# Kernel tuning notes

Hardware: AMD Instinct MI355X
Metric: run time of the kernel (lower is better)

Reference implementation:

```python
import jax, jax.numpy as jnp
import numpy as np

BATCH, NUM_MASKS, IN_DIM, OUT_DIM = 512, 16, 1024, 1024


def setup_inputs() -> dict:
    key = jax.random.key(0)
    k1, k2, k3 = jax.random.split(key, 3)
    x = jax.random.normal(k1, (BATCH, NUM_MASKS, IN_DIM), dtype=jnp.float32)
    kernel = jax.random.normal(k2, (IN_DIM, OUT_DIM), dtype=jnp.float32) * (1.0 / np.sqrt(IN_DIM))
    masks = jax.random.uniform(k3, (NUM_MASKS, IN_DIM, OUT_DIM), dtype=jnp.float32)
    return {"x": x, "kernel": kernel, "masks": masks}


def reference(x, kernel, masks):
    # masked_kernel[m, i, o] = kernel[i, o] * masks[m, i, o]
    masked_kernel = kernel[None, :, :] * masks  # (M, I, O)
    # Original tf.scan serializes batch; equivalent math is one batched einsum:
    # out[b, m, o] = sum_i x[b, m, i] * masked_kernel[m, i, o]
    # NOTE: the executed tf.scan path applies NO activation, so neither do we.
    out = jnp.einsum('bmi,mio->bmo', x, masked_kernel)  # (B, M, O)
    return out
```

## Files before the change

kernel.cpp:

```cpp
#include <hip/hip_runtime.h>
#include <hip/hip_bf16.h>


#define BATCH 512
#define NMASK 16
#define IN_D  1024
#define OUT_D 1024

#define BM 128
#define BN 128
#define BK 32
#define NT (IN_D / BK)
#define AKP 40
#define BKP 34
#define THREADS 512

using bf16x8  = __attribute__((ext_vector_type(8))) __bf16;
using bf16x4t = __attribute__((ext_vector_type(4))) __bf16;
using f32x4   = __attribute__((ext_vector_type(4))) float;
using f32x2   = __attribute__((ext_vector_type(2))) float;
using u16x8   = __attribute__((ext_vector_type(8))) unsigned short;
using u16x4   = __attribute__((ext_vector_type(4))) unsigned short;

__device__ __forceinline__ unsigned short f2bf(float f) {
    unsigned u = __float_as_uint(f);
    u += 0x7fffu + ((u >> 16) & 1u);
    return (unsigned short)(u >> 16);
}

__global__ void __launch_bounds__(THREADS, 4)
mdl_mfma_kernel(const float* __restrict__ X,
                const float* __restrict__ Kn,
                const float* __restrict__ Mk,
                float* __restrict__ Out)
{
    __shared__ __align__(16) unsigned short As[2][BM * AKP];
    __shared__ __align__(16) unsigned short Bs[2][BN * BKP];

    const int t = threadIdx.x;
    const int l = t & 63;
    const int w = t >> 6;

    const int raw = blockIdx.x;
    const int wg  = (raw & 7) * 64 + (raw >> 3);
    const int m   = wg >> 5;
    const int ob  = (wg >> 2) & 7;
    const int bb  = wg & 3;

    const int wr = w >> 2;
    const int wc = w & 3;

    f32x4 acc[4][2];
#pragma unroll
    for (int mi = 0; mi < 4; ++mi)
#pragma unroll
        for (int ni = 0; ni < 2; ++ni)
            acc[mi][ni] = (f32x4){0.f, 0.f, 0.f, 0.f};

    const int a_row = t >> 2;
    const int a_k   = (t & 3) * 8;
    const int o_l = (t & 63) * 2;
    const int ig  = t >> 6;
    const int i_l = ig * 4;

    const float* Xa  = X + ((size_t)(bb * BM + a_row) * NMASK + m) * IN_D + a_k;
    const float* Knb = Kn + (size_t)i_l * OUT_D + ob * BN + o_l;
    const float* Mkb = Mk + ((size_t)m * IN_D + i_l) * OUT_D + ob * BN + o_l;

    f32x4 av0, av1;
    f32x2 kv[4], mv[4];

    auto LOAD = [&](int kt) {
        av0 = *(const f32x4*)(Xa + kt);
        av1 = *(const f32x4*)(Xa + kt + 4);
#pragma unroll
        for (int r = 0; r < 4; ++r) {
            kv[r] = *(const f32x2*)(Knb + (size_t)(kt + r) * OUT_D);
            mv[r] = *(const f32x2*)(Mkb + (size_t)(kt + r) * OUT_D);
        }
    };

    auto STORE = [&](int buf) {
        u16x8 va;
#pragma unroll
        for (int j = 0; j < 4; ++j) { va[j] = f2bf(av0[j]); va[4 + j] = f2bf(av1[j]); }
        *(u16x8*)(&As[buf][a_row * AKP + a_k]) = va;
#pragma unroll
        for (int c = 0; c < 2; ++c) {
            u16x4 v;
#pragma unroll
            for (int r = 0; r < 4; ++r) v[r] = f2bf(kv[r][c] * mv[r][c]);
            *(u16x4*)(&Bs[buf][(o_l + c) * BKP + ig * 4]) = v;
        }
    };

    auto MFMA_PHASE = [&](int buf) {
        const int kg = (l >> 4) * 8;
        bf16x8 af[4], bfv[2];
#pragma unroll
        for (int mi = 0; mi < 4; ++mi) {
            const int r = wr * 64 + mi * 16 + (l & 15);
            af[mi] = *(const bf16x8*)(&As[buf][r * AKP + kg]);
        }
#pragma unroll
        for (int ni = 0; ni < 2; ++ni) {
            const int n = wc * 32 + ni * 16 + (l & 15);
            bf16x4t lo = *(const bf16x4t*)(&Bs[buf][n * BKP + kg]);
            bf16x4t hi = *(const bf16x4t*)(&Bs[buf][n * BKP + kg + 4]);
            bf16x8 f;
            f[0] = lo[0]; f[1] = lo[1]; f[2] = lo[2]; f[3] = lo[3];
            f[4] = hi[0]; f[5] = hi[1]; f[6] = hi[2]; f[7] = hi[3];
            bfv[ni] = f;
        }
#pragma unroll
        for (int mi = 0; mi < 4; ++mi)
#pragma unroll
            for (int ni = 0; ni < 2; ++ni)
                acc[mi][ni] = __builtin_amdgcn_mfma_f32_16x16x32_bf16(
                    af[mi], bfv[ni], acc[mi][ni], 0, 0, 0);
    };

    LOAD(0);
    STORE(0);
    __syncthreads();
    int cur = 0;
    for (int tt = 0; tt < NT; ++tt) {
        if (tt + 1 < NT) {
            LOAD((tt + 1) * BK);
            __builtin_amdgcn_sched_barrier(0);
        }
        MFMA_PHASE(cur);
        if (tt + 1 < NT) STORE(cur ^ 1);
        __syncthreads();
        cur ^= 1;
    }

    const int r0 = bb * BM + wr * 64 + (l >> 4) * 4;
    const int c0 = ob * BN + wc * 32 + (l & 15);
#pragma unroll
    for (int mi = 0; mi < 4; ++mi) {
#pragma unroll
        for (int j = 0; j < 4; ++j) {
            const size_t row = (size_t)(r0 + mi * 16 + j);
            float* op = Out + (row * NMASK + m) * OUT_D + c0;
#pragma unroll
            for (int ni = 0; ni < 2; ++ni)
                op[ni * 16] = acc[mi][ni][j];
        }
    }
}

extern "C" void kernel_launch(void* const* d_in, const int* in_sizes, int n_in,
                              void* d_out, int out_size, void* d_ws, size_t ws_size,
                              hipStream_t stream) {
    (void)in_sizes; (void)n_in; (void)d_ws; (void)ws_size; (void)out_size;
    const float* X  = (const float*)d_in[0];
    const float* Kn = (const float*)d_in[1];
    const float* Mk = (const float*)d_in[2];
    float* Out = (float*)d_out;

    const int nblocks = (BATCH / BM) * (OUT_D / BN) * NMASK;
    mdl_mfma_kernel<<<nblocks, THREADS, 0, stream>>>(X, Kn, Mk, Out);
}
```

Baseline: 52.34 us.

## Prefetch masked-kernel tiles two stages ahead with double register sets and lighter barriers

The global loads for the kernel and mask tiles are now issued two K-tiles ahead into alternating register sets, while X is still prefetched one tile ahead. The loop is unrolled by two so the LDS buffer indices are static. The block barrier is replaced with an explicit lgkmcnt wait plus s_barrier, and the A fragments are loaded per MFMA row instead of all at once. The aim is to hide more of the mask/kernel global-memory latency, at the cost of more VGPRs under launch_bounds(512,4), which may cause spills or reduce occupancy.

```diff
diff --git a/kernel.cpp b/kernel.cpp
--- a/kernel.cpp
+++ b/kernel.cpp
@@ -27,6 +27,8 @@
     u += 0x7fffu + ((u >> 16) & 1u);
     return (unsigned short)(u >> 16);
 }
+
+struct BRegs { f32x2 kv[4]; f32x2 mv[4]; };
 
 __global__ void __launch_bounds__(THREADS, 4)
 mdl_mfma_kernel(const float* __restrict__ X,
@@ -68,40 +70,35 @@
     const float* Mkb = Mk + ((size_t)m * IN_D + i_l) * OUT_D + ob * BN + o_l;
 
     f32x4 av0, av1;
-    f32x2 kv[4], mv[4];
+    BRegs b0, b1;
 
-    auto LOAD = [&](int kt) {
+    auto LOADA = [&](int kt) {
         av0 = *(const f32x4*)(Xa + kt);
         av1 = *(const f32x4*)(Xa + kt + 4);
+    };
+    auto LOADB = [&](BRegs& bg, int kt) {
 #pragma unroll
         for (int r = 0; r < 4; ++r) {
-            kv[r] = *(const f32x2*)(Knb + (size_t)(kt + r) * OUT_D);
-            mv[r] = *(const f32x2*)(Mkb + (size_t)(kt + r) * OUT_D);
+            bg.kv[r] = *(const f32x2*)(Knb + (size_t)(kt + r) * OUT_D);
+            bg.mv[r] = *(const f32x2*)(Mkb + (size_t)(kt + r) * OUT_D);
         }
     };
-
-    auto STORE = [&](int buf) {
+    auto STORE = [&](int buf, BRegs& bg) {
+#pragma unroll
+        for (int c = 0; c < 2; ++c) {
+            u16x4 v;
+#pragma unroll
+            for (int r = 0; r < 4; ++r) v[r] = f2bf(bg.kv[r][c] * bg.mv[r][c]);
+            *(u16x4*)(&Bs[buf][(o_l + c) * BKP + ig * 4]) = v;
+        }
         u16x8 va;
 #pragma unroll
         for (int j = 0; j < 4; ++j) { va[j] = f2bf(av0[j]); va[4 + j] = f2bf(av1[j]); }
         *(u16x8*)(&As[buf][a_row * AKP + a_k]) = va;
-#pragma unroll
-        for (int c = 0; c < 2; ++c) {
-            u16x4 v;
-#pragma unroll
-            for (int r = 0; r < 4; ++r) v[r] = f2bf(kv[r][c] * mv[r][c]);
-            *(u16x4*)(&Bs[buf][(o_l + c) * BKP + ig * 4]) = v;
-        }
     };
-
     auto MFMA_PHASE = [&](int buf) {
         const int kg = (l >> 4) * 8;
-        bf16x8 af[4], bfv[2];
-#pragma unroll
-        for (int mi = 0; mi < 4; ++mi) {
-            const int r = wr * 64 + mi * 16 + (l & 15);
-            af[mi] = *(const bf16x8*)(&As[buf][r * AKP + kg]);
-        }
+        bf16x8 bfv[2];
 #pragma unroll
         for (int ni = 0; ni < 2; ++ni) {
             const int n = wc * 32 + ni * 16 + (l & 15);
@@ -113,26 +110,41 @@
             bfv[ni] = f;
         }
 #pragma unroll
-        for (int mi = 0; mi < 4; ++mi)
+        for (int mi = 0; mi < 4; ++mi) {
+            const int r = wr * 64 + mi * 16 + (l & 15);
+            bf16x8 af = *(const bf16x8*)(&As[buf][r * AKP + kg]);
 #pragma unroll
             for (int ni = 0; ni < 2; ++ni)
                 acc[mi][ni] = __builtin_amdgcn_mfma_f32_16x16x32_bf16(
-                    af[mi], bfv[ni], acc[mi][ni], 0, 0, 0);
+                    af, bfv[ni], acc[mi][ni], 0, 0, 0);
+        }
+    };
+    auto BARRIER = [&]() {
+        asm volatile("s_waitcnt lgkmcnt(0)" ::: "memory");
+        __builtin_amdgcn_sched_barrier(0);
+        __builtin_amdgcn_s_barrier();
+        __builtin_amdgcn_sched_barrier(0);
     };
 
-    LOAD(0);
-    STORE(0);
-    __syncthreads();
-    int cur = 0;
-    for (int tt = 0; tt < NT; ++tt) {
-        if (tt + 1 < NT) {
-            LOAD((tt + 1) * BK);
-            __builtin_amdgcn_sched_barrier(0);
-        }
-        MFMA_PHASE(cur);
-        if (tt + 1 < NT) STORE(cur ^ 1);
-        __syncthreads();
-        cur ^= 1;
+    LOADA(0);
+    LOADB(b0, 0);
+    STORE(0, b0);
+    LOADB(b1, BK);
+    BARRIER();
+
+    for (int tt = 0; tt < NT; tt += 2) {
+        if (tt + 1 < NT) LOADA((tt + 1) * BK);
+        if (tt + 2 < NT) LOADB(b0, (tt + 2) * BK);
+        __builtin_amdgcn_sched_barrier(0);
+        MFMA_PHASE(0);
+        if (tt + 1 < NT) STORE(1, b1);
+        BARRIER();
+        if (tt + 2 < NT) LOADA((tt + 2) * BK);
+        if (tt + 3 < NT) LOADB(b1, (tt + 3) * BK);
+        __builtin_amdgcn_sched_barrier(0);
+        MFMA_PHASE(1);
+        if (tt + 2 < NT) STORE(0, b0);
+        BARRIER();
     }
 
     const int r0 = bb * BM + wr * 64 + (l >> 4) * 4;
```

New measurement: 56.90 us. +8.7%, slower.

## Use 256x128 tiles with 32x32x16 MFMA and XOR-swizzled LDS layout

Applied to the files above, without the earlier changes.

Doubles the batch tile to 256 rows so each block reuses the masked-kernel tile (kernel*mask product and its loads) across twice as many rows, halving mask/kernel global traffic and conversion work. Switches from 16x16x32 to 32x32x16 bf16 MFMA with 64x64 per-wave tiles, and replaces the padded B layout with an XOR-swizzled layout allowing single 16-byte LDS reads. The plain syncthreads is replaced by an explicit lgkmcnt wait plus s_barrier. Costs more registers and LDS per block and halves the grid to 256 blocks, which may reduce occupancy.

```diff
diff --git a/kernel.cpp b/kernel.cpp
--- a/kernel.cpp
+++ b/kernel.cpp
@@ -7,26 +7,18 @@
 #define IN_D  1024
 #define OUT_D 1024
 
-#define BM 128
+#define BM 256
 #define BN 128
 #define BK 32
 #define NT (IN_D / BK)
 #define AKP 40
-#define BKP 34
 #define THREADS 512
 
-using bf16x8  = __attribute__((ext_vector_type(8))) __bf16;
-using bf16x4t = __attribute__((ext_vector_type(4))) __bf16;
-using f32x4   = __attribute__((ext_vector_type(4))) float;
-using f32x2   = __attribute__((ext_vector_type(2))) float;
-using u16x8   = __attribute__((ext_vector_type(8))) unsigned short;
-using u16x4   = __attribute__((ext_vector_type(4))) unsigned short;
-
-__device__ __forceinline__ unsigned short f2bf(float f) {
-    unsigned u = __float_as_uint(f);
-    u += 0x7fffu + ((u >> 16) & 1u);
-    return (unsigned short)(u >> 16);
-}
+using bf16x8 = __attribute__((ext_vector_type(8))) __bf16;
+using bf16x4 = __attribute__((ext_vector_type(4))) __bf16;
+using f32x16 = __attribute__((ext_vector_type(16))) float;
+using f32x4  = __attribute__((ext_vector_type(4))) float;
+using f32x2  = __attribute__((ext_vector_type(2))) float;
 
 __global__ void __launch_bounds__(THREADS, 4)
 mdl_mfma_kernel(const float* __restrict__ X,
@@ -35,44 +27,48 @@
                 float* __restrict__ Out)
 {
     __shared__ __align__(16) unsigned short As[2][BM * AKP];
-    __shared__ __align__(16) unsigned short Bs[2][BN * BKP];
+    __shared__ __align__(16) unsigned short Bs[2][BN * AKP];
 
     const int t = threadIdx.x;
     const int l = t & 63;
     const int w = t >> 6;
 
     const int raw = blockIdx.x;
-    const int wg  = (raw & 7) * 64 + (raw >> 3);
-    const int m   = wg >> 5;
-    const int ob  = (wg >> 2) & 7;
-    const int bb  = wg & 3;
+    const int wg  = (raw & 7) * 32 + (raw >> 3);
+    const int m   = wg >> 4;
+    const int ob  = (wg >> 1) & 7;
+    const int bb  = wg & 1;
 
-    const int wr = w >> 2;
-    const int wc = w & 3;
+    const int wrow = (w >> 1) * 64;
+    const int wcol = (w & 1) * 64;
 
-    f32x4 acc[4][2];
+    f32x16 acc[2][2];
 #pragma unroll
-    for (int mi = 0; mi < 4; ++mi)
+    for (int ti = 0; ti < 2; ++ti)
 #pragma unroll
-        for (int ni = 0; ni < 2; ++ni)
-            acc[mi][ni] = (f32x4){0.f, 0.f, 0.f, 0.f};
+        for (int tj = 0; tj < 2; ++tj)
+#pragma unroll
+            for (int e = 0; e < 16; ++e)
+                acc[ti][tj][e] = 0.f;
 
-    const int a_row = t >> 2;
-    const int a_k   = (t & 3) * 8;
-    const int o_l = (t & 63) * 2;
-    const int ig  = t >> 6;
-    const int i_l = ig * 4;
+    const int a_row = t >> 1;
+    const int a_kh  = (t & 1) * 16;
+    const int a_x   = (a_row >> 3) & 3;
+    const int a_p0  = (t & 1) * 2;
+    const int o2  = (t & 63) * 2;
+    const int kq  = w * 4;
 
-    const float* Xa  = X + ((size_t)(bb * BM + a_row) * NMASK + m) * IN_D + a_k;
-    const float* Knb = Kn + (size_t)i_l * OUT_D + ob * BN + o_l;
-    const float* Mkb = Mk + ((size_t)m * IN_D + i_l) * OUT_D + ob * BN + o_l;
+    const float* Xa  = X + ((size_t)(bb * BM + a_row) * NMASK + m) * IN_D + a_kh;
+    const float* Knb = Kn + (size_t)kq * OUT_D + ob * BN + o2;
+    const float* Mkb = Mk + ((size_t)m * IN_D + kq) * OUT_D + ob * BN + o2;
 
-    f32x4 av0, av1;
+    f32x4 av[4];
     f32x2 kv[4], mv[4];
 
     auto LOAD = [&](int kt) {
-        av0 = *(const f32x4*)(Xa + kt);
-        av1 = *(const f32x4*)(Xa + kt + 4);
+#pragma unroll
+        for (int j = 0; j < 4; ++j)
+            av[j] = *(const f32x4*)(Xa + kt + j * 4);
 #pragma unroll
         for (int r = 0; r < 4; ++r) {
             kv[r] = *(const f32x2*)(Knb + (size_t)(kt + r) * OUT_D);
@@ -81,71 +77,89 @@
     };
 
     auto STORE = [&](int buf) {
-        u16x8 va;
-#pragma unroll
-        for (int j = 0; j < 4; ++j) { va[j] = f2bf(av0[j]); va[4 + j] = f2bf(av1[j]); }
-        *(u16x8*)(&As[buf][a_row * AKP + a_k]) = va;
 #pragma unroll
         for (int c = 0; c < 2; ++c) {
-            u16x4 v;
+            const int o  = o2 + c;
+            const int xb = (o >> 3) & 3;
+            bf16x4 v;
 #pragma unroll
-            for (int r = 0; r < 4; ++r) v[r] = f2bf(kv[r][c] * mv[r][c]);
-            *(u16x4*)(&Bs[buf][(o_l + c) * BKP + ig * 4]) = v;
+            for (int r = 0; r < 4; ++r)
+                v[r] = (__bf16)(kv[r][c] * mv[r][c]);
+            *(bf16x4*)(&Bs[buf][o * AKP + (((w >> 1) ^ xb) * 8) + (w & 1) * 4]) = v;
+        }
+        bf16x8 va0, va1;
+#pragma unroll
+        for (int j = 0; j < 4; ++j) {
+            va0[j] = (__bf16)av[0][j];  va0[4 + j] = (__bf16)av[1][j];
+            va1[j] = (__bf16)av[2][j];  va1[4 + j] = (__bf16)av[3][j];
+        }
+        *(bf16x8*)(&As[buf][a_row * AKP + ((a_p0 ^ a_x) * 8)])       = va0;
+        *(bf16x8*)(&As[buf][a_row * AKP + (((a_p0 + 1) ^ a_x) * 8)]) = va1;
+    };
+
+    auto MFMA_PHASE = [&](int buf) {
+#pragma unroll
+        for (int s = 0; s < 2; ++s) {
+            const int p = s * 2 + (l >> 5);
+            bf16x8 af[2], bfv[2];
+#pragma unroll
+            for (int ti = 0; ti < 2; ++ti) {
+                const int r  = wrow + ti * 32 + (l & 31);
+                const int xa = (r >> 3) & 3;
+                af[ti] = *(const bf16x8*)(&As[buf][r * AKP + ((p ^ xa) * 8)]);
+            }
+#pragma unroll
+            for (int tj = 0; tj < 2; ++tj) {
+                const int o  = wcol + tj * 32 + (l & 31);
+                const int xb = (o >> 3) & 3;
+                bfv[tj] = *(const bf16x8*)(&Bs[buf][o * AKP + ((p ^ xb) * 8)]);
+            }
+#pragma unroll
+            for (int ti = 0; ti < 2; ++ti)
+#pragma unroll
+                for (int tj = 0; tj < 2; ++tj)
+                    acc[ti][tj] = __builtin_amdgcn_mfma_f32_32x32x16_bf16(
+                        af[ti], bfv[tj], acc[ti][tj], 0, 0, 0);
         }
     };
 
-    auto MFMA_PHASE = [&](int buf) {
-        const int kg = (l >> 4) * 8;
-        bf16x8 af[4], bfv[2];
-#pragma unroll
-        for (int mi = 0; mi < 4; ++mi) {
-            const int r = wr * 64 + mi * 16 + (l & 15);
-            af[mi] = *(const bf16x8*)(&As[buf][r * AKP + kg]);
-        }
-#pragma unroll
-        for (int ni = 0; ni < 2; ++ni) {
-            const int n = wc * 32 + ni * 16 + (l & 15);
-            bf16x4t lo = *(const bf16x4t*)(&Bs[buf][n * BKP + kg]);
-            bf16x4t hi = *(const bf16x4t*)(&Bs[buf][n * BKP + kg + 4]);
-            bf16x8 f;
-            f[0] = lo[0]; f[1] = lo[1]; f[2] = lo[2]; f[3] = lo[3];
-            f[4] = hi[0]; f[5] = hi[1]; f[6] = hi[2]; f[7] = hi[3];
-            bfv[ni] = f;
-        }
-#pragma unroll
-        for (int mi = 0; mi < 4; ++mi)
-#pragma unroll
-            for (int ni = 0; ni < 2; ++ni)
-                acc[mi][ni] = __builtin_amdgcn_mfma_f32_16x16x32_bf16(
-                    af[mi], bfv[ni], acc[mi][ni], 0, 0, 0);
+    auto BARRIER = [&]() {
+        asm volatile("s_waitcnt lgkmcnt(0)" ::: "memory");
+        __builtin_amdgcn_sched_barrier(0);
+        __builtin_amdgcn_s_barrier();
+        __builtin_amdgcn_sched_barrier(0);
     };
 
     LOAD(0);
     STORE(0);
-    __syncthreads();
-    int cur = 0;
+    BARRIER();
+
     for (int tt = 0; tt < NT; ++tt) {
+        const int cur = tt & 1;
         if (tt + 1 < NT) {
             LOAD((tt + 1) * BK);
             __builtin_amdgcn_sched_barrier(0);
         }
         MFMA_PHASE(cur);
         if (tt + 1 < NT) STORE(cur ^ 1);
-        __syncthreads();
-        cur ^= 1;
+        BARRIER();
     }
 
-    const int r0 = bb * BM + wr * 64 + (l >> 4) * 4;
-    const int c0 = ob * BN + wc * 32 + (l & 15);
+    const int r0 = bb * BM + wrow + 4 * (l >> 5);
+    const int c0 = ob * BN + wcol + (l & 31);
 #pragma unroll
-    for (int mi = 0; mi < 4; ++mi) {
+    for (int ti = 0; ti < 2; ++ti) {
 #pragma unroll
-        for (int j = 0; j < 4; ++j) {
-            const size_t row = (size_t)(r0 + mi * 16 + j);
-            float* op = Out + (row * NMASK + m) * OUT_D + c0;
+        for (int tj = 0; tj < 2; ++tj) {
 #pragma unroll
-            for (int ni = 0; ni < 2; ++ni)
-                op[ni * 16] = acc[mi][ni][j];
+            for (int g = 0; g < 4; ++g) {
+#pragma unroll
+                for (int q = 0; q < 4; ++q) {
+                    const int row = r0 + ti * 32 + g * 8 + q;
+                    const int col = c0 + tj * 32;
+                    Out[((size_t)row * NMASK + m) * OUT_D + col] = acc[ti][tj][g * 4 + q];
+                }
+            }
         }
     }
 }
```

Measured after the change: 56.68 us. +8.3%, slower.

## Stream mask tiles via global_load_lds DMA and restructure pipeline

Applied to the files above, without the earlier changes.

Mask tiles are now copied straight from global memory into an fp32 shared-memory staging buffer with global_load_lds, double-buffered one tile ahead. X and kernel loads are issued at the start of each iteration and converted in the same iteration, so they are no longer prefetched. The masked product and bf16 conversion now read masks from LDS, and a second barrier per iteration is added. The aim is to cut vector-register pressure and issue cost for the large mask stream, at the price of 32KB of extra LDS (which may lower occupancy) and X/kernel load latency exposed inside the loop.

```diff
diff --git a/kernel.cpp b/kernel.cpp
--- a/kernel.cpp
+++ b/kernel.cpp
@@ -15,17 +15,17 @@
 #define BKP 34
 #define THREADS 512
 
-using bf16x8  = __attribute__((ext_vector_type(8))) __bf16;
-using bf16x4t = __attribute__((ext_vector_type(4))) __bf16;
-using f32x4   = __attribute__((ext_vector_type(4))) float;
-using f32x2   = __attribute__((ext_vector_type(2))) float;
-using u16x8   = __attribute__((ext_vector_type(8))) unsigned short;
-using u16x4   = __attribute__((ext_vector_type(4))) unsigned short;
+using bf16x8 = __attribute__((ext_vector_type(8))) __bf16;
+using bf16x4 = __attribute__((ext_vector_type(4))) __bf16;
+using f32x4  = __attribute__((ext_vector_type(4))) float;
+using f32x2  = __attribute__((ext_vector_type(2))) float;
 
-__device__ __forceinline__ unsigned short f2bf(float f) {
-    unsigned u = __float_as_uint(f);
-    u += 0x7fffu + ((u >> 16) & 1u);
-    return (unsigned short)(u >> 16);
+typedef const __attribute__((address_space(1))) void gvoid_t;
+typedef __attribute__((address_space(3))) void lvoid_t;
+
+__device__ __forceinline__ void dma16(const void* g, const void* l) {
+    __builtin_amdgcn_global_load_lds((gvoid_t*)(uintptr_t)g,
+                                     (lvoid_t*)(uintptr_t)l, 16, 0, 0);
 }
 
 __global__ void __launch_bounds__(THREADS, 4)
@@ -34,6 +34,7 @@
                 const float* __restrict__ Mk,
                 float* __restrict__ Out)
 {
+    __shared__ __align__(16) float          Mf[2][BK * BN];
     __shared__ __align__(16) unsigned short As[2][BM * AKP];
     __shared__ __align__(16) unsigned short Bs[2][BN * BKP];
 
@@ -58,81 +59,103 @@
             acc[mi][ni] = (f32x4){0.f, 0.f, 0.f, 0.f};
 
     const int a_row = t >> 2;
-    const int a_k   = (t & 3) * 8;
-    const int o_l = (t & 63) * 2;
-    const int ig  = t >> 6;
-    const int i_l = ig * 4;
+    const int a_kh  = (t & 3) * 8;
+    const int o2 = (t & 63) * 2;
+    const int k4 = w * 4;
 
-    const float* Xa  = X + ((size_t)(bb * BM + a_row) * NMASK + m) * IN_D + a_k;
-    const float* Knb = Kn + (size_t)i_l * OUT_D + ob * BN + o_l;
-    const float* Mkb = Mk + ((size_t)m * IN_D + i_l) * OUT_D + ob * BN + o_l;
+    const int obase = ob * BN;
+    const float* Xa  = X + ((size_t)(bb * BM + a_row) * NMASK + m) * IN_D + a_kh;
+    const float* Knb = Kn + obase + o2;
+    const float* Mkm = Mk + (size_t)m * IN_D * OUT_D;
 
-    f32x4 av0, av1;
-    f32x2 kv[4], mv[4];
-
-    auto LOAD = [&](int kt) {
-        av0 = *(const f32x4*)(Xa + kt);
-        av1 = *(const f32x4*)(Xa + kt + 4);
+    auto DMA = [&](int tile, int buf) {
+        const int kt = tile * BK;
 #pragma unroll
-        for (int r = 0; r < 4; ++r) {
-            kv[r] = *(const f32x2*)(Knb + (size_t)(kt + r) * OUT_D);
-            mv[r] = *(const f32x2*)(Mkb + (size_t)(kt + r) * OUT_D);
-        }
-    };
-
-    auto STORE = [&](int buf) {
-        u16x8 va;
-#pragma unroll
-        for (int j = 0; j < 4; ++j) { va[j] = f2bf(av0[j]); va[4 + j] = f2bf(av1[j]); }
-        *(u16x8*)(&As[buf][a_row * AKP + a_k]) = va;
-#pragma unroll
-        for (int c = 0; c < 2; ++c) {
-            u16x4 v;
-#pragma unroll
-            for (int r = 0; r < 4; ++r) v[r] = f2bf(kv[r][c] * mv[r][c]);
-            *(u16x4*)(&Bs[buf][(o_l + c) * BKP + ig * 4]) = v;
+        for (int j = 0; j < 2; ++j) {
+            const int k = j * 16 + w * 2 + (l >> 5);
+            const float* gsrc = Mkm + (size_t)(kt + k) * OUT_D + obase + (l & 31) * 4;
+            const float* ldst = &Mf[buf][j * 2048 + w * 256];
+            dma16(gsrc, ldst);
         }
     };
 
     auto MFMA_PHASE = [&](int buf) {
         const int kg = (l >> 4) * 8;
-        bf16x8 af[4], bfv[2];
-#pragma unroll
-        for (int mi = 0; mi < 4; ++mi) {
-            const int r = wr * 64 + mi * 16 + (l & 15);
-            af[mi] = *(const bf16x8*)(&As[buf][r * AKP + kg]);
-        }
+        bf16x8 bfv[2];
 #pragma unroll
         for (int ni = 0; ni < 2; ++ni) {
             const int n = wc * 32 + ni * 16 + (l & 15);
-            bf16x4t lo = *(const bf16x4t*)(&Bs[buf][n * BKP + kg]);
-            bf16x4t hi = *(const bf16x4t*)(&Bs[buf][n * BKP + kg + 4]);
+            bf16x4 lo = *(const bf16x4*)(&Bs[buf][n * BKP + kg]);
+            bf16x4 hi = *(const bf16x4*)(&Bs[buf][n * BKP + kg + 4]);
             bf16x8 f;
             f[0] = lo[0]; f[1] = lo[1]; f[2] = lo[2]; f[3] = lo[3];
             f[4] = hi[0]; f[5] = hi[1]; f[6] = hi[2]; f[7] = hi[3];
             bfv[ni] = f;
         }
 #pragma unroll
-        for (int mi = 0; mi < 4; ++mi)
+        for (int mi = 0; mi < 4; ++mi) {
+            const int r = wr * 64 + mi * 16 + (l & 15);
+            bf16x8 af = *(const bf16x8*)(&As[buf][r * AKP + kg]);
 #pragma unroll
             for (int ni = 0; ni < 2; ++ni)
                 acc[mi][ni] = __builtin_amdgcn_mfma_f32_16x16x32_bf16(
-                    af[mi], bfv[ni], acc[mi][ni], 0, 0, 0);
+                    af, bfv[ni], acc[mi][ni], 0, 0, 0);
+        }
     };
 
-    LOAD(0);
-    STORE(0);
-    __syncthreads();
-    int cur = 0;
+    DMA(0, 0);
+    asm volatile("s_waitcnt vmcnt(0)" ::: "memory");
+    __builtin_amdgcn_s_barrier();
+    __builtin_amdgcn_sched_barrier(0);
+
     for (int tt = 0; tt < NT; ++tt) {
-        if (tt + 1 < NT) {
-            LOAD((tt + 1) * BK);
-            __builtin_amdgcn_sched_barrier(0);
+        const int cur = tt & 1;
+        const int kt  = tt * BK;
+
+        f32x4 xv0 = *(const f32x4*)(Xa + kt);
+        f32x4 xv1 = *(const f32x4*)(Xa + kt + 4);
+        f32x2 kv[4];
+#pragma unroll
+        for (int r = 0; r < 4; ++r)
+            kv[r] = *(const f32x2*)(Knb + (size_t)(kt + k4 + r) * OUT_D);
+        __builtin_amdgcn_sched_barrier(0);
+
+        if (tt + 1 < NT) DMA(tt + 1, cur ^ 1);
+        __builtin_amdgcn_sched_barrier(0);
+
+        {
+            f32x2 mvv[4];
+#pragma unroll
+            for (int r = 0; r < 4; ++r)
+                mvv[r] = *(const f32x2*)(&Mf[cur][(k4 + r) * BN + o2]);
+#pragma unroll
+            for (int c = 0; c < 2; ++c) {
+                bf16x4 v;
+#pragma unroll
+                for (int r = 0; r < 4; ++r)
+                    v[r] = (__bf16)(kv[r][c] * mvv[r][c]);
+                *(bf16x4*)(&Bs[cur][(o2 + c) * BKP + k4]) = v;
+            }
+            bf16x8 va;
+#pragma unroll
+            for (int j = 0; j < 4; ++j) {
+                va[j]     = (__bf16)xv0[j];
+                va[4 + j] = (__bf16)xv1[j];
+            }
+            *(bf16x8*)(&As[cur][a_row * AKP + a_kh]) = va;
         }
+
+        asm volatile("s_waitcnt lgkmcnt(0)" ::: "memory");
+        __builtin_amdgcn_sched_barrier(0);
+        __builtin_amdgcn_s_barrier();
+        __builtin_amdgcn_sched_barrier(0);
+
         MFMA_PHASE(cur);
-        if (tt + 1 < NT) STORE(cur ^ 1);
-        __syncthreads();
-        cur ^= 1;
+
+        asm volatile("s_waitcnt vmcnt(0)" ::: "memory");
+        __builtin_amdgcn_sched_barrier(0);
+        __builtin_amdgcn_s_barrier();
+        __builtin_amdgcn_sched_barrier(0);
     }
 
     const int r0 = bb * BM + wr * 64 + (l >> 4) * 4;
```

New measurement: 52.19 us. No clear change (-0.3%).
